# Performance work log

Hardware: AMD Instinct MI355X
Metric: run time of the kernel (lower is better)

Reference implementation:

```python
import jax, jax.numpy as jnp
import numpy as np

N_VERT = 40962  # icosphere level-6 vertex count
K = 7           # 1-ring neighborhood size (self + 6 neighbors)


def setup_inputs() -> dict:
    key = jax.random.key(0)
    k1, k2, k3 = jax.random.split(key, 3)
    x = jax.random.normal(k1, (16, 256, N_VERT), dtype=jnp.float32)
    neigh_orders = jax.random.randint(k2, (N_VERT * K,), 0, N_VERT, dtype=jnp.int32)
    W = jax.random.normal(k3, (1, 2 * K), dtype=jnp.float32) * 0.1  # Linear(14 -> 1) weight
    b = jnp.zeros((1,), dtype=jnp.float32)
    return {"x": x, "neigh_orders": neigh_orders, "W": W, "b": b}


def reference(x, neigh_orders, W, b):
    # x: [B, C, N] features on spherical mesh vertices
    avg = jnp.mean(x, axis=1, keepdims=True)          # [B, 1, N] (AdaptiveAvgPool2d((1,None)))
    mx = jnp.max(x, axis=1, keepdims=True)            # [B, 1, N] (AdaptiveMaxPool2d((1,None)))
    pool = jnp.concatenate([avg, mx], axis=1)         # [B, 2, N]
    p = jnp.transpose(pool, (0, 2, 1))                # [B, N, 2]
    idx = neigh_orders.reshape(N_VERT, K)             # [N, 7] 1-ring neighbor indices
    g = p[:, idx, :]                                  # [B, N, 7, 2] neighbor gather
    g = g.reshape(p.shape[0], N_VERT, 2 * K)          # [B, N, 14]
    out = jnp.einsum('bnf,of->bno', g, W) + b         # [B, N, 1] Linear(14 -> 1)
    att = jax.nn.sigmoid(out)
    return jnp.transpose(att, (0, 2, 1))              # [B, 1, N] spatial attention map
```

## Files before the change

kernel.cpp:

```cpp
#include <hip/hip_runtime.h>
#include <math.h>

#define B_DIM 16
#define C_DIM 256
#define NV    40962
#define K_NEI 7

__global__ void pool_kernel(const float* __restrict__ x, float4* __restrict__ pool) {
    const int NPAIR = NV / 2;
    int t = blockIdx.x * blockDim.x + threadIdx.x;
    if (t >= B_DIM * NPAIR) return;
    int b  = t / NPAIR;
    int n2 = t - b * NPAIR;

    const float* xb = x + (size_t)b * C_DIM * NV + 2 * (size_t)n2;

    float sx = 0.f, sy = 0.f;
    float mx = -INFINITY, my = -INFINITY;
    #pragma unroll 8
    for (int c = 0; c < C_DIM; ++c) {
        float2 v = *reinterpret_cast<const float2*>(xb + (size_t)c * NV);
        sx += v.x; sy += v.y;
        mx = fmaxf(mx, v.x);
        my = fmaxf(my, v.y);
    }
    const float inv = 1.0f / (float)C_DIM;
    float4 o;
    o.x = sx * inv; o.y = mx;
    o.z = sy * inv; o.w = my;
    pool[((size_t)b * NV + 2 * (size_t)n2) >> 1] = o;
}

__global__ void att_kernel(const float2* __restrict__ pool,
                           const int* __restrict__ idx,
                           const float* __restrict__ W,
                           const float* __restrict__ bias,
                           float* __restrict__ out) {
    int t = blockIdx.x * blockDim.x + threadIdx.x;
    if (t >= B_DIM * NV) return;
    int b = t / NV;
    int n = t - b * NV;

    const float2* pb = pool + (size_t)b * NV;
    float acc = bias[0];
    #pragma unroll
    for (int k = 0; k < K_NEI; ++k) {
        int j = idx[n * K_NEI + k];
        float2 am = pb[j];
        acc = fmaf(W[2 * k], am.x, acc);
        acc = fmaf(W[2 * k + 1], am.y, acc);
    }
    out[t] = 1.0f / (1.0f + expf(-acc));
}

extern "C" void kernel_launch(void* const* d_in, const int* in_sizes, int n_in,
                              void* d_out, int out_size, void* d_ws, size_t ws_size,
                              hipStream_t stream) {
    const float* x     = (const float*)d_in[0];
    const int*   neigh = (const int*)  d_in[1];
    const float* W     = (const float*)d_in[2];
    const float* bias  = (const float*)d_in[3];
    float*       out   = (float*)d_out;

    float4* pool4 = (float4*)d_ws;

    const int NPAIR = NV / 2;
    int t1 = B_DIM * NPAIR;
    pool_kernel<<<(t1 + 255) / 256, 256, 0, stream>>>(x, pool4);

    int t2 = B_DIM * NV;
    att_kernel<<<(t2 + 255) / 256, 256, 0, stream>>>((const float2*)d_ws, neigh, W, bias, out);
}
```

Baseline: 142.6 us.

## Transpose pooled features to vertex-major layout and use non-temporal streaming loads

Adds a transpose kernel that turns the pooled [B,N,2] buffer into [N,B,2]. A new attention kernel then gathers one contiguous row per neighbor and computes all 16 batches per thread. The pooling loop switches to non-temporal loads with a higher unroll factor. This aims to cut scattered gather traffic and cache pollution from streaming x. In exchange it adds an extra kernel launch and a transpose pass, and the new kernel runs at low occupancy. The new path is taken only when the workspace is large enough.

After: 136.2 us. -4.5%, faster.

```diff
diff --git a/kernel.cpp b/kernel.cpp
--- a/kernel.cpp
+++ b/kernel.cpp
@@ -5,9 +5,11 @@
 #define C_DIM 256
 #define NV    40962
 #define K_NEI 7
+#define NPAIR (NV / 2)
+
+typedef float v2f __attribute__((ext_vector_type(2)));
 
 __global__ void pool_kernel(const float* __restrict__ x, float4* __restrict__ pool) {
-    const int NPAIR = NV / 2;
     int t = blockIdx.x * blockDim.x + threadIdx.x;
     if (t >= B_DIM * NPAIR) return;
     int b  = t / NPAIR;
@@ -17,9 +19,10 @@
 
     float sx = 0.f, sy = 0.f;
     float mx = -INFINITY, my = -INFINITY;
-    #pragma unroll 8
+    #pragma unroll 16
     for (int c = 0; c < C_DIM; ++c) {
-        float2 v = *reinterpret_cast<const float2*>(xb + (size_t)c * NV);
+        v2f v = __builtin_nontemporal_load(
+                    reinterpret_cast<const v2f*>(xb + (size_t)c * NV));
         sx += v.x; sy += v.y;
         mx = fmaxf(mx, v.x);
         my = fmaxf(my, v.y);
@@ -29,6 +32,65 @@
     o.x = sx * inv; o.y = mx;
     o.z = sy * inv; o.w = my;
     pool[((size_t)b * NV + 2 * (size_t)n2) >> 1] = o;
+}
+
+__global__ void transpose_kernel(const float2* __restrict__ pool,
+                                 float2* __restrict__ poolT) {
+    __shared__ float2 tile[64][17];
+    int n0 = blockIdx.x * 64;
+    int i  = threadIdx.x & 63;
+    int bq = threadIdx.x >> 6;
+    #pragma unroll
+    for (int p = 0; p < 4; ++p) {
+        int b = p * 4 + bq;
+        if (n0 + i < NV)
+            tile[i][b] = pool[(size_t)b * NV + n0 + i];
+    }
+    __syncthreads();
+    int valid = NV - n0; if (valid > 64) valid = 64;
+    int nf4 = valid * 8;
+    float4* dst = reinterpret_cast<float4*>(poolT + (size_t)n0 * 16);
+    for (int e = threadIdx.x; e < nf4; e += 256) {
+        int e2 = e * 2;
+        int n  = e2 >> 4;
+        int b  = e2 & 15;
+        float2 a0 = tile[n][b];
+        float2 a1 = tile[n][b + 1];
+        dst[e] = make_float4(a0.x, a0.y, a1.x, a1.y);
+    }
+}
+
+__global__ void att2_kernel(const float2* __restrict__ poolT,
+                            const int* __restrict__ idx,
+                            const float* __restrict__ W,
+                            const float* __restrict__ bias,
+                            float* __restrict__ out) {
+    int n = blockIdx.x * 64 + threadIdx.x;
+    if (n >= NV) return;
+
+    float w[2 * K_NEI];
+    #pragma unroll
+    for (int i = 0; i < 2 * K_NEI; ++i) w[i] = W[i];
+    float bb = bias[0];
+
+    float acc[16];
+    #pragma unroll
+    for (int b = 0; b < 16; ++b) acc[b] = bb;
+
+    #pragma unroll
+    for (int k = 0; k < K_NEI; ++k) {
+        int j = idx[n * K_NEI + k];
+        const float4* L = reinterpret_cast<const float4*>(poolT + (size_t)j * 16);
+        #pragma unroll
+        for (int q = 0; q < 8; ++q) {
+            float4 v = L[q];
+            acc[2 * q]     = fmaf(w[2 * k + 1], v.y, fmaf(w[2 * k], v.x, acc[2 * q]));
+            acc[2 * q + 1] = fmaf(w[2 * k + 1], v.w, fmaf(w[2 * k], v.z, acc[2 * q + 1]));
+        }
+    }
+    #pragma unroll
+    for (int b = 0; b < 16; ++b)
+        out[(size_t)b * NV + n] = 1.0f / (1.0f + expf(-acc[b]));
 }
 
 __global__ void att_kernel(const float2* __restrict__ pool,
@@ -62,12 +124,20 @@
     const float* bias  = (const float*)d_in[3];
     float*       out   = (float*)d_out;
 
+    const size_t POOL_BYTES = (size_t)B_DIM * NV * sizeof(float2);
+
     float4* pool4 = (float4*)d_ws;
-
-    const int NPAIR = NV / 2;
     int t1 = B_DIM * NPAIR;
     pool_kernel<<<(t1 + 255) / 256, 256, 0, stream>>>(x, pool4);
 
-    int t2 = B_DIM * NV;
-    att_kernel<<<(t2 + 255) / 256, 256, 0, stream>>>((const float2*)d_ws, neigh, W, bias, out);
+    if (ws_size >= 2 * POOL_BYTES) {
+        float2* poolT = (float2*)((char*)d_ws + POOL_BYTES);
+        int ntile = (NV + 63) / 64;
+        transpose_kernel<<<ntile, 256, 0, stream>>>((const float2*)d_ws, poolT);
+        att2_kernel<<<ntile, 64, 0, stream>>>(poolT, neigh, W, bias, out);
+    } else {
+        int t2 = B_DIM * NV;
+        att_kernel<<<(t2 + 255) / 256, 256, 0, stream>>>((const float2*)d_ws,
+                                                         neigh, W, bias, out);
+    }
 }
```

## Transpose pooled buffer to vertex-major and compute all batches per thread in attention

Applied to the files above, without the earlier changes.

The pooled mean/max buffer is now stored vertex-major with the 16 batches contiguous per vertex. The attention kernel assigns one thread per vertex and loops over all batches, so each neighbor index is loaded once and the 128-byte neighbor row is read with float4 loads. The pool kernel also switches to nontemporal loads and a larger unroll. The trade-offs are scattered stores in the pool kernel, a small 641-block grid of 64 threads for the attention kernel, and higher register pressure.

Measured after the change: 140.3 us. About the same (-1.6%).

```diff
diff --git a/kernel.cpp b/kernel.cpp
--- a/kernel.cpp
+++ b/kernel.cpp
@@ -5,9 +5,11 @@
 #define C_DIM 256
 #define NV    40962
 #define K_NEI 7
+#define NPAIR (NV / 2)
 
-__global__ void pool_kernel(const float* __restrict__ x, float4* __restrict__ pool) {
-    const int NPAIR = NV / 2;
+typedef float v2f __attribute__((ext_vector_type(2)));
+
+__global__ void pool_kernel(const float* __restrict__ x, float2* __restrict__ poolT) {
     int t = blockIdx.x * blockDim.x + threadIdx.x;
     if (t >= B_DIM * NPAIR) return;
     int b  = t / NPAIR;
@@ -17,40 +19,52 @@
 
     float sx = 0.f, sy = 0.f;
     float mx = -INFINITY, my = -INFINITY;
-    #pragma unroll 8
+    #pragma unroll 16
     for (int c = 0; c < C_DIM; ++c) {
-        float2 v = *reinterpret_cast<const float2*>(xb + (size_t)c * NV);
+        v2f v = __builtin_nontemporal_load(
+                    reinterpret_cast<const v2f*>(xb + (size_t)c * NV));
         sx += v.x; sy += v.y;
         mx = fmaxf(mx, v.x);
         my = fmaxf(my, v.y);
     }
     const float inv = 1.0f / (float)C_DIM;
-    float4 o;
-    o.x = sx * inv; o.y = mx;
-    o.z = sy * inv; o.w = my;
-    pool[((size_t)b * NV + 2 * (size_t)n2) >> 1] = o;
+
+    size_t n = 2 * (size_t)n2;
+    poolT[n * 16 + b]       = make_float2(sx * inv, mx);
+    poolT[(n + 1) * 16 + b] = make_float2(sy * inv, my);
 }
 
-__global__ void att_kernel(const float2* __restrict__ pool,
-                           const int* __restrict__ idx,
-                           const float* __restrict__ W,
-                           const float* __restrict__ bias,
-                           float* __restrict__ out) {
-    int t = blockIdx.x * blockDim.x + threadIdx.x;
-    if (t >= B_DIM * NV) return;
-    int b = t / NV;
-    int n = t - b * NV;
+__global__ void att2_kernel(const float2* __restrict__ poolT,
+                            const int* __restrict__ idx,
+                            const float* __restrict__ W,
+                            const float* __restrict__ bias,
+                            float* __restrict__ out) {
+    int n = blockIdx.x * 64 + threadIdx.x;
+    if (n >= NV) return;
 
-    const float2* pb = pool + (size_t)b * NV;
-    float acc = bias[0];
+    float w[2 * K_NEI];
+    #pragma unroll
+    for (int i = 0; i < 2 * K_NEI; ++i) w[i] = W[i];
+    float bb = bias[0];
+
+    float acc[16];
+    #pragma unroll
+    for (int b = 0; b < 16; ++b) acc[b] = bb;
+
     #pragma unroll
     for (int k = 0; k < K_NEI; ++k) {
         int j = idx[n * K_NEI + k];
-        float2 am = pb[j];
-        acc = fmaf(W[2 * k], am.x, acc);
-        acc = fmaf(W[2 * k + 1], am.y, acc);
+        const float4* L = reinterpret_cast<const float4*>(poolT + (size_t)j * 16);
+        #pragma unroll
+        for (int q = 0; q < 8; ++q) {
+            float4 v = L[q];
+            acc[2 * q]     = fmaf(w[2 * k + 1], v.y, fmaf(w[2 * k], v.x, acc[2 * q]));
+            acc[2 * q + 1] = fmaf(w[2 * k + 1], v.w, fmaf(w[2 * k], v.z, acc[2 * q + 1]));
+        }
     }
-    out[t] = 1.0f / (1.0f + expf(-acc));
+    #pragma unroll
+    for (int b = 0; b < 16; ++b)
+        out[(size_t)b * NV + n] = 1.0f / (1.0f + expf(-acc[b]));
 }
 
 extern "C" void kernel_launch(void* const* d_in, const int* in_sizes, int n_in,
@@ -62,12 +76,11 @@
     const float* bias  = (const float*)d_in[3];
     float*       out   = (float*)d_out;
 
-    float4* pool4 = (float4*)d_ws;
+    float2* poolT = (float2*)d_ws;
 
-    const int NPAIR = NV / 2;
     int t1 = B_DIM * NPAIR;
-    pool_kernel<<<(t1 + 255) / 256, 256, 0, stream>>>(x, pool4);
+    pool_kernel<<<(t1 + 255) / 256, 256, 0, stream>>>(x, poolT);
 
-    int t2 = B_DIM * NV;
-    att_kernel<<<(t2 + 255) / 256, 256, 0, stream>>>((const float2*)d_ws, neigh, W, bias, out);
+    int ntile = (NV + 63) / 64;
+    att2_kernel<<<ntile, 64, 0, stream>>>(poolT, neigh, W, bias, out);
 }
```
